# Kernel optimization log

Measured on AMD Instinct MI355X. Metric: run time of the kernel, lower is better.

Reference implementation:

```python
import jax, jax.numpy as jnp
import numpy as np

B, G, P = 4096, 31, 8
C = P * (P + 1) // 2  # 36 pairwise-with-replacement combinations


def setup_inputs() -> dict:
    key = jax.random.key(0)
    k1, k2 = jax.random.split(key)
    param_tensor = jax.random.normal(k1, (B, G, G, P), dtype=jnp.float32)
    integral_coeffs = jax.random.normal(k2, (G, G, C), dtype=jnp.float32)
    return {"param_tensor": param_tensor, "integral_coeffs": integral_coeffs}


def reference(param_tensor, integral_coeffs):
    # torch.combinations(param, 2, with_replacement=True).prod(-1) over last dim
    # == param[ii] * param[jj] for upper-triangular-with-diagonal index pairs.
    P_ = param_tensor.shape[-1]
    ii, jj = np.triu_indices(P_)  # same ordering as torch.combinations with_replacement
    pairs = param_tensor[..., ii] * param_tensor[..., jj]  # [B, G, G, C]
    # weight by per-cell coeffs, sum over pair dim and over both grid dims -> [B]
    return jnp.einsum('bghc,ghc->b', pairs, integral_coeffs)
```

## Files before the change

### kernel.cpp

```cpp
#include <hip/hip_runtime.h>

#define B_  4096
#define G_  31
#define GG_ 961
#define P_  8
#define C_  36
#define R_  16
#define CH_ 4

typedef float floatx4 __attribute__((ext_vector_type(4)));

__global__ void zero_kernel(float* out, int n) {
    int i = blockIdx.x * blockDim.x + threadIdx.x;
    if (i < n) out[i] = 0.0f;
}

__global__ __launch_bounds__(256, 3)
void quadform_kernel(const float* __restrict__ param,
                     const float* __restrict__ coef,
                     float* __restrict__ out) {
    const int lane    = threadIdx.x & 63;
    const int wv      = threadIdx.x >> 6;
    const int gh_tile = blockIdx.x * 4 + wv;
    const int gh      = gh_tile * 64 + lane;
    const bool valid  = gh < GG_;
    const int  ghc    = valid ? gh : (GG_ - 1);

    const int b0 = blockIdx.y * R_;
    const floatx4* pb = reinterpret_cast<const floatx4*>(param);
    const size_t base  = ((size_t)b0 * GG_ + ghc) * 2;
    const size_t bstep = (size_t)GG_ * 2;

    floatx4 qA[CH_][2], qB[CH_][2];

#define LOADC(Q, CHK)                                                          \
    {                                                                          \
        _Pragma("unroll")                                                      \
        for (int r = 0; r < CH_; ++r) {                                        \
            const floatx4* p_ = pb + base + (size_t)((CHK) * CH_ + r) * bstep; \
            Q[r][0] = __builtin_nontemporal_load(p_);                          \
            Q[r][1] = __builtin_nontemporal_load(p_ + 1);                      \
        }                                                                      \
    }

    LOADC(qA, 0);
    LOADC(qB, 1);

    float cf[C_];
    {
        const floatx4* cp = reinterpret_cast<const floatx4*>(coef) + (size_t)ghc * (C_ / 4);
        #pragma unroll
        for (int q = 0; q < C_ / 4; ++q) {
            floatx4 v = cp[q];
            cf[4*q+0] = v.x; cf[4*q+1] = v.y; cf[4*q+2] = v.z; cf[4*q+3] = v.w;
        }
    }
    if (!valid) {
        #pragma unroll
        for (int c = 0; c < C_; ++c) cf[c] = 0.0f;
    }

    float s[R_];

#define DO_CHUNK(Q, S0)                                                        \
    {                                                                          \
        _Pragma("unroll")                                                      \
        for (int r = 0; r < CH_; ++r) {                                        \
            const float pv[P_] = {Q[r][0].x, Q[r][0].y, Q[r][0].z, Q[r][0].w,  \
                                  Q[r][1].x, Q[r][1].y, Q[r][1].z, Q[r][1].w}; \
            float acc = 0.0f;                                                  \
            int c = 0;                                                         \
            _Pragma("unroll")                                                  \
            for (int i = 0; i < P_; ++i) {                                     \
                float t = 0.0f;                                                \
                _Pragma("unroll")                                              \
                for (int j = i; j < P_; ++j) { t = fmaf(cf[c], pv[j], t); ++c; } \
                acc = fmaf(pv[i], t, acc);                                     \
            }                                                                  \
            s[(S0) + r] = acc;                                                 \
        }                                                                      \
    }

    DO_CHUNK(qA, 0);
    LOADC(qA, 2);
    DO_CHUNK(qB, 4);
    LOADC(qB, 3);
    DO_CHUNK(qA, 8);
    DO_CHUNK(qB, 12);

    #pragma unroll
    for (int off = 32; off; off >>= 1) {
        #pragma unroll
        for (int r = 0; r < R_; ++r) s[r] += __shfl_xor(s[r], off, 64);
    }

    __shared__ float red[4][R_];
    if (lane == 0) {
        #pragma unroll
        for (int r = 0; r < R_; ++r) red[wv][r] = s[r];
    }
    __syncthreads();
    if (threadIdx.x < R_) {
        const int r = threadIdx.x;
        float v = red[0][r] + red[1][r] + red[2][r] + red[3][r];
        atomicAdd(&out[b0 + r], v);
    }
}

extern "C" void kernel_launch(void* const* d_in, const int* in_sizes, int n_in,
                              void* d_out, int out_size, void* d_ws, size_t ws_size,
                              hipStream_t stream) {
    const float* param = (const float*)d_in[0];
    const float* coef  = (const float*)d_in[1];
    float* out = (float*)d_out;

    zero_kernel<<<(B_ + 255) / 256, 256, 0, stream>>>(out, B_);

    dim3 grid(4, B_ / R_);
    quadform_kernel<<<grid, 256, 0, stream>>>(param, coef, out);
}
```

Measured before the change: 176.4 us.

## Have each block cover the full grid for 8 batches, dropping atomics and the zero kernel

Each block now handles 8 batch rows and loops over all four 256-cell tiles of the 961-cell grid, instead of splitting the grid across four blocks with atomic accumulation. This removes the separate zero-init launch and the atomicAdd, and writes the output directly. Coefficient and parameter loads are double-buffered across tiles so the next tile's loads overlap the current tile's arithmetic. Launch bounds drop to 2 blocks per SM because of the higher register use, which may reduce occupancy for this bandwidth-bound kernel.

```diff
diff --git a/kernel.cpp b/kernel.cpp
--- a/kernel.cpp
+++ b/kernel.cpp
@@ -5,64 +5,73 @@
 #define GG_ 961
 #define P_  8
 #define C_  36
-#define R_  16
+#define R_  8
 #define CH_ 4
+#define NT_ 4
 
 typedef float floatx4 __attribute__((ext_vector_type(4)));
 
-__global__ void zero_kernel(float* out, int n) {
-    int i = blockIdx.x * blockDim.x + threadIdx.x;
-    if (i < n) out[i] = 0.0f;
-}
-
-__global__ __launch_bounds__(256, 3)
+__global__ __launch_bounds__(256, 2)
 void quadform_kernel(const float* __restrict__ param,
                      const float* __restrict__ coef,
                      float* __restrict__ out) {
-    const int lane    = threadIdx.x & 63;
-    const int wv      = threadIdx.x >> 6;
-    const int gh_tile = blockIdx.x * 4 + wv;
-    const int gh      = gh_tile * 64 + lane;
-    const bool valid  = gh < GG_;
-    const int  ghc    = valid ? gh : (GG_ - 1);
+    const int lane = threadIdx.x & 63;
+    const int wv   = threadIdx.x >> 6;
+    const int b0   = blockIdx.x * R_;
 
-    const int b0 = blockIdx.y * R_;
     const floatx4* pb = reinterpret_cast<const floatx4*>(param);
-    const size_t base  = ((size_t)b0 * GG_ + ghc) * 2;
     const size_t bstep = (size_t)GG_ * 2;
 
-    floatx4 qA[CH_][2], qB[CH_][2];
+    size_t base[NT_]; bool val[NT_]; int ghc[NT_];
+    #pragma unroll
+    for (int t = 0; t < NT_; ++t) {
+        int gh = (t * 4 + wv) * 64 + lane;
+        val[t]  = gh < GG_;
+        ghc[t]  = val[t] ? gh : (GG_ - 1);
+        base[t] = ((size_t)b0 * GG_ + ghc[t]) * 2;
+    }
 
-#define LOADC(Q, CHK)                                                          \
+    floatx4 qA[2][CH_][2];
+    floatx4 qB[CH_][2];
+    float   cfb[2][C_];
+
+#define LOADA(BUF, T)                                                          \
     {                                                                          \
         _Pragma("unroll")                                                      \
         for (int r = 0; r < CH_; ++r) {                                        \
-            const floatx4* p_ = pb + base + (size_t)((CHK) * CH_ + r) * bstep; \
-            Q[r][0] = __builtin_nontemporal_load(p_);                          \
-            Q[r][1] = __builtin_nontemporal_load(p_ + 1);                      \
+            const floatx4* p_ = pb + base[T] + (size_t)r * bstep;              \
+            qA[BUF][r][0] = __builtin_nontemporal_load(p_);                    \
+            qA[BUF][r][1] = __builtin_nontemporal_load(p_ + 1);                \
         }                                                                      \
     }
 
-    LOADC(qA, 0);
-    LOADC(qB, 1);
-
-    float cf[C_];
-    {
-        const floatx4* cp = reinterpret_cast<const floatx4*>(coef) + (size_t)ghc * (C_ / 4);
-        #pragma unroll
-        for (int q = 0; q < C_ / 4; ++q) {
-            floatx4 v = cp[q];
-            cf[4*q+0] = v.x; cf[4*q+1] = v.y; cf[4*q+2] = v.z; cf[4*q+3] = v.w;
-        }
-    }
-    if (!valid) {
-        #pragma unroll
-        for (int c = 0; c < C_; ++c) cf[c] = 0.0f;
+#define LOADB(T)                                                               \
+    {                                                                          \
+        _Pragma("unroll")                                                      \
+        for (int r = 0; r < CH_; ++r) {                                        \
+            const floatx4* p_ = pb + base[T] + (size_t)(CH_ + r) * bstep;      \
+            qB[r][0] = __builtin_nontemporal_load(p_);                         \
+            qB[r][1] = __builtin_nontemporal_load(p_ + 1);                     \
+        }                                                                      \
     }
 
-    float s[R_];
+#define LOADCF(BUF, T)                                                         \
+    {                                                                          \
+        const floatx4* cp = reinterpret_cast<const floatx4*>(coef)             \
+                            + (size_t)ghc[T] * (C_ / 4);                       \
+        _Pragma("unroll")                                                      \
+        for (int q = 0; q < C_ / 4; ++q) {                                     \
+            floatx4 v = cp[q];                                                 \
+            cfb[BUF][4*q+0] = v.x; cfb[BUF][4*q+1] = v.y;                      \
+            cfb[BUF][4*q+2] = v.z; cfb[BUF][4*q+3] = v.w;                      \
+        }                                                                      \
+        if (!val[T]) {                                                         \
+            _Pragma("unroll")                                                  \
+            for (int c = 0; c < C_; ++c) cfb[BUF][c] = 0.0f;                   \
+        }                                                                      \
+    }
 
-#define DO_CHUNK(Q, S0)                                                        \
+#define DO_CHUNK(Q, CF, S0)                                                    \
     {                                                                          \
         _Pragma("unroll")                                                      \
         for (int r = 0; r < CH_; ++r) {                                        \
@@ -72,21 +81,33 @@
             int c = 0;                                                         \
             _Pragma("unroll")                                                  \
             for (int i = 0; i < P_; ++i) {                                     \
-                float t = 0.0f;                                                \
+                float tsum = 0.0f;                                             \
                 _Pragma("unroll")                                              \
-                for (int j = i; j < P_; ++j) { t = fmaf(cf[c], pv[j], t); ++c; } \
-                acc = fmaf(pv[i], t, acc);                                     \
+                for (int j = i; j < P_; ++j) {                                 \
+                    tsum = fmaf(CF[c], pv[j], tsum); ++c;                      \
+                }                                                              \
+                acc = fmaf(pv[i], tsum, acc);                                  \
             }                                                                  \
-            s[(S0) + r] = acc;                                                 \
+            s[(S0) + r] += acc;                                                \
         }                                                                      \
     }
 
-    DO_CHUNK(qA, 0);
-    LOADC(qA, 2);
-    DO_CHUNK(qB, 4);
-    LOADC(qB, 3);
-    DO_CHUNK(qA, 8);
-    DO_CHUNK(qB, 12);
+    float s[R_];
+    #pragma unroll
+    for (int r = 0; r < R_; ++r) s[r] = 0.0f;
+
+    LOADCF(0, 0);
+    LOADA(0, 0);
+
+    #pragma unroll
+    for (int t = 0; t < NT_; ++t) {
+        const int cur = t & 1, nxt = cur ^ 1;
+        LOADB(t);
+        if (t < NT_ - 1) LOADCF(nxt, t + 1);
+        DO_CHUNK(qA[cur], cfb[cur], 0);
+        if (t < NT_ - 1) LOADA(nxt, t + 1);
+        DO_CHUNK(qB, cfb[cur], 4);
+    }
 
     #pragma unroll
     for (int off = 32; off; off >>= 1) {
@@ -102,8 +123,7 @@
     __syncthreads();
     if (threadIdx.x < R_) {
         const int r = threadIdx.x;
-        float v = red[0][r] + red[1][r] + red[2][r] + red[3][r];
-        atomicAdd(&out[b0 + r], v);
+        out[b0 + r] = red[0][r] + red[1][r] + red[2][r] + red[3][r];
     }
 }
 
@@ -114,8 +134,5 @@
     const float* coef  = (const float*)d_in[1];
     float* out = (float*)d_out;
 
-    zero_kernel<<<(B_ + 255) / 256, 256, 0, stream>>>(out, B_);
-
-    dim3 grid(4, B_ / R_);
-    quadform_kernel<<<grid, 256, 0, stream>>>(param, coef, out);
+    quadform_kernel<<<dim3(B_ / R_), 256, 0, stream>>>(param, coef, out);
 }
```

Result: slower. 210.5 us (+19.3%).
